# Kernel tuning notes

Measured on AMD Instinct MI355X. Metric: run time of the kernel, lower is better.

The kernel has to match this reference:

```python
import jax, jax.numpy as jnp
import numpy as np

EPS = 1e-4
HEADS = 8
DIM_HEAD = 32
BALANCE = 0.3


def _normalize(x, dims):
    # torch normalize(): norm over `dims` in fp32; norm = eps + norm*sqrt(norm.numel()/x.numel())
    red = 1
    for d in dims:
        red *= x.shape[d]
    norm = jnp.sqrt(jnp.sum(jnp.square(x.astype(jnp.float32)), axis=dims, keepdims=True))
    norm = EPS + norm / np.sqrt(red)
    return x / norm.astype(x.dtype)


def _mpconv1x1(x, w, gain=1.0):
    # MPConv forward (eval mode): weight-normalize per output channel, scale, 1x1 conv
    w = w.astype(jnp.float32)
    w = _normalize(w, (1, 2, 3))
    fan_in = w.shape[1] * w.shape[2] * w.shape[3]
    w = (w * (gain / np.sqrt(fan_in))).astype(x.dtype)[:, :, 0, 0]  # [out, in]
    return jnp.einsum('oi,nihw->nohw', w, x)


def setup_inputs() -> dict:
    key = jax.random.key(0)
    k1, k2, k3 = jax.random.split(key, 3)
    x = jax.random.normal(k1, (2, 256, 48, 48), dtype=jnp.float32)
    w_qkv = jax.random.normal(k2, (768, 256, 1, 1), dtype=jnp.float32)
    w_out = jax.random.normal(k3, (256, 256, 1, 1), dtype=jnp.float32)
    return {"x": x, "w_qkv": w_qkv, "w_out": w_out}


def reference(x, w_qkv, w_out):
    n, c, h, w_sp = x.shape
    seq = h * w_sp
    y = _mpconv1x1(x, w_qkv)                          # [n, 3c, h, w]
    y = y.reshape(n, HEADS, DIM_HEAD, 3, seq)         # channel split: head x dim_head x 3
    y = _normalize(y, (2,))                           # L2-normalize over dim_head axis
    q = y[:, :, :, 0, :]
    k = y[:, :, :, 1, :]
    v = y[:, :, :, 2, :]
    # scores [n, h, q, k] with k scaled by 1/sqrt(dim_head)
    att = jax.nn.softmax(jnp.einsum('nhcq,nhck->nhqk', q, k) / np.sqrt(DIM_HEAD), axis=3)
    y = jnp.einsum('nhqk,nhck->nhcq', att, v)         # [n, heads, dim_head, seq]
    y = _mpconv1x1(y.reshape(n, c, h, w_sp), w_out)
    t = BALANCE
    # mp_sum: lerp then magnitude-preserving rescale
    return (x + t * (y - x)) / np.sqrt((1 - t) ** 2 + t ** 2)
```

## Files before the change

### kernel.cpp

```cpp
#include <hip/hip_runtime.h>
#include <math.h>

#define EPSN 1e-4f
#define SEQ 2304

using bf16x8 = __attribute__((ext_vector_type(8))) short;
using f32x4  = __attribute__((ext_vector_type(4))) float;

__device__ inline unsigned short f2bf(float x) {
    union { float f; unsigned u; } c; c.f = x;
    unsigned u = c.u;
    u += 0x7fffu + ((u >> 16) & 1u);
    return (unsigned short)(u >> 16);
}

__device__ inline unsigned cvt_pk_bf16(float lo, float hi) {
    unsigned r;
    asm("v_cvt_pk_bf16_f32 %0, %1, %2" : "=v"(r) : "v"(lo), "v"(hi));
    return r;
}
__device__ inline void permlane32_swap(unsigned &a, unsigned &b) {
    asm("v_permlane32_swap_b32 %0, %1" : "+v"(a), "+v"(b));
}
__device__ inline void permlane16_swap(unsigned &a, unsigned &b) {
    asm("v_permlane16_swap_b32 %0, %1" : "+v"(a), "+v"(b));
}

__global__ __launch_bounds__(256) void prep_w_kernel(const float* __restrict__ w_qkv,
                                                     const float* __restrict__ w_out,
                                                     unsigned short* __restrict__ wqb,
                                                     unsigned short* __restrict__ wob) {
    int wave = threadIdx.x >> 6, lane = threadIdx.x & 63;
    int row = blockIdx.x * 4 + wave;
    const float* src;
    unsigned short* dst;
    if (row < 768) { src = w_qkv + (size_t)row * 256; dst = wqb + (size_t)row * 256; }
    else           { src = w_out + (size_t)(row - 768) * 256; dst = wob + (size_t)(row - 768) * 256; }
    float4 v = *(const float4*)&src[lane * 4];
    float ss = v.x * v.x + v.y * v.y + v.z * v.z + v.w * v.w;
    for (int off = 32; off > 0; off >>= 1) ss += __shfl_xor(ss, off, 64);
    float sc = 1.0f / (sqrtf(ss) + 16.0f * EPSN);
    unsigned p0 = (unsigned)f2bf(v.x * sc) | ((unsigned)f2bf(v.y * sc) << 16);
    unsigned p1 = (unsigned)f2bf(v.z * sc) | ((unsigned)f2bf(v.w * sc) << 16);
    *(uint2*)&dst[lane * 4] = make_uint2(p0, p1);
}

__global__ __launch_bounds__(256) void qkv_fused_kernel(const float* __restrict__ x,
                                                        const unsigned short* __restrict__ wqb,
                                                        unsigned short* __restrict__ qn,
                                                        unsigned short* __restrict__ kn,
                                                        unsigned short* __restrict__ vn) {
    __shared__ __align__(16) unsigned short Xs[32][264];
    __shared__ float Cs[96][33];
    __shared__ __align__(16) unsigned short Vls[32][40];
    int bid = blockIdx.x;
    int xcd = bid & 7, j = bid >> 3;
    int h = j & 7;
    int tile = xcd * 18 + (j >> 3);
    int st2 = tile % 72, n = tile / 72;
    int tid = threadIdx.x;
    int wave = tid >> 6, lane = tid & 63;
    int ln = lane & 15, quad = lane >> 4;
    int sgrp = wave & 1, mgrp = wave >> 1;
    int s0 = st2 * 32;

    {
        int ci = tid >> 3, sv = (tid & 7) * 4;
#pragma unroll
        for (int p = 0; p < 8; ++p) {
            int c = p * 32 + ci;
            float4 v = *(const float4*)&x[(size_t)(n * 256 + c) * SEQ + s0 + sv];
            Xs[sv + 0][c] = f2bf(v.x);
            Xs[sv + 1][c] = f2bf(v.y);
            Xs[sv + 2][c] = f2bf(v.z);
            Xs[sv + 3][c] = f2bf(v.w);
        }
    }
    __syncthreads();

    const unsigned short* Abase = wqb + (size_t)(h * 96 + mgrp * 48 + ln) * 256 + quad * 8;
    f32x4 acc[3];
#pragma unroll
    for (int m = 0; m < 3; ++m) acc[m] = (f32x4){0.f, 0.f, 0.f, 0.f};
#pragma unroll
    for (int kc = 0; kc < 8; ++kc) {
        bf16x8 b = *(const bf16x8*)&Xs[sgrp * 16 + ln][kc * 32 + quad * 8];
#pragma unroll
        for (int m = 0; m < 3; ++m) {
            bf16x8 a = *(const bf16x8*)(Abase + (size_t)(m * 16) * 256 + kc * 32);
            acc[m] = __builtin_amdgcn_mfma_f32_16x16x32_bf16(a, b, acc[m], 0, 0, 0);
        }
    }
#pragma unroll
    for (int m = 0; m < 3; ++m)
#pragma unroll
        for (int r = 0; r < 4; ++r)
            Cs[mgrp * 48 + m * 16 + quad * 4 + r][sgrp * 16 + ln] = acc[m][r];
    __syncthreads();
    int nh = n * 8 + h;
    if (tid < 96) {
        int sl = tid & 31, wh = tid >> 5;
        int s = st2 * 32 + sl;
        float v[32];
        float ss = 0.f;
#pragma unroll
        for (int d = 0; d < 32; ++d) { v[d] = Cs[3 * d + wh][sl]; ss += v[d] * v[d]; }
        float inv = 1.0f / (EPSN + sqrtf(ss * (1.0f / 32.0f)));
        if (wh == 0) inv *= 0.17677669529663687f * 1.4426950408889634f;
        if (wh == 2) {
#pragma unroll
            for (int d = 0; d < 32; ++d) Vls[d][sl] = f2bf(v[d] * inv);
        } else {
            unsigned short* dst = (wh == 1 ? kn : qn) + (size_t)nh * 73728 + (size_t)s * 32;
            unsigned wbuf[16];
#pragma unroll
            for (int j2 = 0; j2 < 16; ++j2)
                wbuf[j2] = (unsigned)f2bf(v[2 * j2] * inv) | ((unsigned)f2bf(v[2 * j2 + 1] * inv) << 16);
#pragma unroll
            for (int j2 = 0; j2 < 4; ++j2) {
                uint4 t4 = make_uint4(wbuf[4 * j2], wbuf[4 * j2 + 1], wbuf[4 * j2 + 2], wbuf[4 * j2 + 3]);
                *(uint4*)(dst + j2 * 8) = t4;
            }
        }
    }
    __syncthreads();
    {
        int d = tid >> 3, sj = (tid & 7) * 4;
        uint2 t2 = *(const uint2*)&Vls[d][sj];
        *(uint2*)&vn[(size_t)nh * 73728 + (size_t)d * SEQ + st2 * 32 + sj] = t2;
    }
}

__global__ __launch_bounds__(256) void attn_mfma_kernel(const unsigned short* __restrict__ qn,
                                                        const unsigned short* __restrict__ kn,
                                                        const unsigned short* __restrict__ vn,
                                                        float* __restrict__ Opart,
                                                        float* __restrict__ Lpart) {
    __shared__ __align__(16) unsigned short Ks[2][64][40];
    __shared__ __align__(16) unsigned short Vs[2][32][72];
    int tid = threadIdx.x;
    int wq = tid >> 6, lane = tid & 63;
    int ln = lane & 15, quad = lane >> 4;
    int bid = blockIdx.x;
    int xcd = bid & 7, bi = bid >> 3;
    int nh = xcd * 2 + (bi >= 144);
    int bi2 = (bi >= 144) ? bi - 144 : bi;
    int qt = bi2 % 36, kz = bi2 / 36;
    const unsigned short* Qg = qn + (size_t)nh * 73728;
    const unsigned short* Kg = kn + (size_t)nh * 73728;
    const unsigned short* Vg = vn + (size_t)nh * 73728;

    bf16x8 qf = *(const bf16x8*)(Qg + (size_t)(qt * 64 + wq * 16 + ln) * 32 + quad * 8);
    bf16x8 ones;
#pragma unroll
    for (int i = 0; i < 8; ++i) ones[i] = (short)0x3F80;

    f32x4 o0 = {0.f, 0.f, 0.f, 0.f};
    f32x4 o1 = {0.f, 0.f, 0.f, 0.f};
    f32x4 lac = {0.f, 0.f, 0.f, 0.f};

    const int NT = 9;
    int s0 = kz * NT * 64;

    auto compute_tile = [&](int bsel) {
        const f32x4 zero = {0.f, 0.f, 0.f, 0.f};
        unsigned w[4][2];
#pragma unroll
        for (int c = 0; c < 4; ++c) {
            bf16x8 kf = *(const bf16x8*)(&Ks[bsel][c * 16 + ln][quad * 8]);
            f32x4 sc = __builtin_amdgcn_mfma_f32_16x16x32_bf16(kf, qf, zero, 0, 0, 0);
            w[c][0] = cvt_pk_bf16(exp2f(sc[0]), exp2f(sc[1]));
            w[c][1] = cvt_pk_bf16(exp2f(sc[2]), exp2f(sc[3]));
        }
#pragma unroll
        for (int kc = 0; kc < 2; ++kc) {
            unsigned a0 = w[2 * kc][0], b0 = w[2 * kc + 1][0];
            permlane32_swap(a0, b0);
            permlane16_swap(a0, b0);
            unsigned a1 = w[2 * kc][1], b1 = w[2 * kc + 1][1];
            permlane32_swap(a1, b1);
            permlane16_swap(a1, b1);
            union { unsigned u[4]; bf16x8 v8; } pk;
            pk.u[0] = a0; pk.u[1] = a1; pk.u[2] = b0; pk.u[3] = b1;
            bf16x8 v0 = *(const bf16x8*)(&Vs[bsel][ln][kc * 32 + quad * 8]);
            bf16x8 v1 = *(const bf16x8*)(&Vs[bsel][16 + ln][kc * 32 + quad * 8]);
            lac = __builtin_amdgcn_mfma_f32_16x16x32_bf16(pk.v8, ones, lac, 0, 0, 0);
            o0  = __builtin_amdgcn_mfma_f32_16x16x32_bf16(pk.v8, v0, o0, 0, 0, 0);
            o1  = __builtin_amdgcn_mfma_f32_16x16x32_bf16(pk.v8, v1, o1, 0, 0, 0);
        }
    };

    uint4 kA = *(const uint4*)(Kg + (size_t)s0 * 32 + tid * 8);
    uint4 vA = *(const uint4*)(Vg + (size_t)(tid >> 3) * SEQ + s0 + (tid & 7) * 8);
    *(uint4*)(&Ks[0][tid >> 2][(tid & 3) * 8]) = kA;
    *(uint4*)(&Vs[0][tid >> 3][(tid & 7) * 8]) = vA;
    uint4 kB = *(const uint4*)(Kg + (size_t)(s0 + 64) * 32 + tid * 8);
    uint4 vB = *(const uint4*)(Vg + (size_t)(tid >> 3) * SEQ + (s0 + 64) + (tid & 7) * 8);

    for (int i = 0; i < NT; i += 2) {
        if (i + 2 < NT) {
            int sn = s0 + (i + 2) * 64;
            kA = *(const uint4*)(Kg + (size_t)sn * 32 + tid * 8);
            vA = *(const uint4*)(Vg + (size_t)(tid >> 3) * SEQ + sn + (tid & 7) * 8);
        }
        __syncthreads();
        compute_tile(0);
        if (i + 1 < NT) {
            *(uint4*)(&Ks[1][tid >> 2][(tid & 3) * 8]) = kB;
            *(uint4*)(&Vs[1][tid >> 3][(tid & 7) * 8]) = vB;
        }
        if (i + 3 < NT) {
            int sn = s0 + (i + 3) * 64;
            kB = *(const uint4*)(Kg + (size_t)sn * 32 + tid * 8);
            vB = *(const uint4*)(Vg + (size_t)(tid >> 3) * SEQ + sn + (tid & 7) * 8);
        }
        __syncthreads();
        if (i + 1 < NT) compute_tile(1);
        if (i + 2 < NT) {
            *(uint4*)(&Ks[0][tid >> 2][(tid & 3) * 8]) = kA;
            *(uint4*)(&Vs[0][tid >> 3][(tid & 7) * 8]) = vA;
        }
    }

    float* Ob = Opart + ((size_t)(kz * 16 + nh) * 36 + qt) * 2048;
    float* Lb = Lpart + ((size_t)(kz * 16 + nh) * 36 + qt) * 64;
#pragma unroll
    for (int r = 0; r < 4; ++r) {
        int ql = wq * 16 + quad * 4 + r;
        Ob[ql * 32 + ln]      = o0[r];
        Ob[ql * 32 + 16 + ln] = o1[r];
        if (ln == 0) Lb[ql] = lac[r];
    }
}

__global__ __launch_bounds__(256) void out_gemm_kernel(const float* __restrict__ Opart,
                                                       const float* __restrict__ Lpart,
                                                       const unsigned short* __restrict__ wob,
                                                       const float* __restrict__ x,
                                                       float* __restrict__ out) {
    __shared__ float Linv[8][16];
    __shared__ __align__(16) unsigned short Ys[16][264];
    int bid = blockIdx.x;
    int xcd = bid & 7, j = bid >> 3;
    int mt = j & 3;
    int u = j >> 2;
    int n = u & 1;
    int st = xcd * 18 + (u >> 1);
    int qt = st >> 2;
    int qo = (st & 3) * 16;
    int tid = threadIdx.x;

    if (tid < 128) {
        int h = tid >> 4, qi = tid & 15;
        size_t base = ((size_t)((n * 8 + h) * 36) + qt) * 64 + qo + qi;
        const size_t kzs = (size_t)16 * 36 * 64;
        float l = Lpart[base] + Lpart[base + kzs] + Lpart[base + 2 * kzs] + Lpart[base + 3 * kzs];
        Linv[h][qi] = 1.0f / l;
    }
    __syncthreads();
    {
        int qi = tid >> 4, dp = tid & 15, d0 = dp * 2;
        const size_t kzs = (size_t)16 * 36 * 2048;
#pragma unroll
        for (int h = 0; h < 8; ++h) {
            size_t ob = ((size_t)((n * 8 + h) * 36) + qt) * 2048 + (size_t)(qo + qi) * 32 + d0;
            float2 a = *(const float2*)&Opart[ob];
            float2 b = *(const float2*)&Opart[ob + kzs];
            float2 e = *(const float2*)&Opart[ob + 2 * kzs];
            float2 f = *(const float2*)&Opart[ob + 3 * kzs];
            float li = Linv[h][qi];
            float r0 = ((a.x + b.x) + (e.x + f.x)) * li;
            float r1 = ((a.y + b.y) + (e.y + f.y)) * li;
            *(unsigned*)&Ys[qi][h * 32 + d0] = cvt_pk_bf16(r0, r1);
        }
    }
    __syncthreads();

    int wave = tid >> 6, lane = tid & 63;
    int ln = lane & 15, quad = lane >> 4;
    int m0 = mt * 64 + wave * 16;
    const unsigned short* Abase = wob + (size_t)(m0 + ln) * 256 + quad * 8;
    f32x4 acc = (f32x4){0.f, 0.f, 0.f, 0.f};
#pragma unroll
    for (int kc = 0; kc < 8; ++kc) {
        bf16x8 a = *(const bf16x8*)(Abase + kc * 32);
        bf16x8 b = *(const bf16x8*)&Ys[ln][kc * 32 + quad * 8];
        acc = __builtin_amdgcn_mfma_f32_16x16x32_bf16(a, b, acc, 0, 0, 0);
    }
    const float c0f = 0.7f * 1.3130643285972254f;
    const float c1f = 0.3f * 1.3130643285972254f;
#pragma unroll
    for (int r = 0; r < 4; ++r) {
        int o = m0 + quad * 4 + r;
        int s = st * 16 + ln;
        size_t idx = (size_t)(n * 256 + o) * SEQ + s;
        out[idx] = c0f * x[idx] + c1f * acc[r];
    }
}

extern "C" void kernel_launch(void* const* d_in, const int* in_sizes, int n_in,
                              void* d_out, int out_size, void* d_ws, size_t ws_size,
                              hipStream_t stream) {
    (void)in_sizes; (void)n_in; (void)out_size; (void)ws_size;
    const float* x     = (const float*)d_in[0];
    const float* w_qkv = (const float*)d_in[1];
    const float* w_out = (const float*)d_in[2];
    float* out = (float*)d_out;
    float* ws  = (float*)d_ws;
    unsigned short* wqb = (unsigned short*)(ws);
    unsigned short* wob = (unsigned short*)(ws + 98304);
    unsigned short* qn  = (unsigned short*)(ws + 131072);
    unsigned short* kn  = (unsigned short*)(ws + 720896);
    unsigned short* vn  = (unsigned short*)(ws + 1310720);
    float* Opart = ws + 1900544;
    float* Lpart = ws + 6619136;

    hipLaunchKernelGGL(prep_w_kernel, dim3(256), dim3(256), 0, stream,
                       w_qkv, w_out, wqb, wob);
    hipLaunchKernelGGL(qkv_fused_kernel, dim3(1152), dim3(256), 0, stream,
                       x, wqb, qn, kn, vn);
    hipLaunchKernelGGL(attn_mfma_kernel, dim3(2304), dim3(256), 0, stream,
                       qn, kn, vn, Opart, Lpart);
    hipLaunchKernelGGL(out_gemm_kernel, dim3(1152), dim3(256), 0, stream,
                       Opart, Lpart, wob, x, out);
}
```

Before: 123.3 us.

## Load K/V fragments directly from global memory, dropping LDS double buffering

The attention kernel no longer stages K and V tiles through double-buffered shared memory with barriers. Each lane now reads its MFMA K and V fragments straight from global memory, relying on L1/L2 caching, since all four waves read the same K/V data. This removes LDS writes, reads and __syncthreads, but each wave now issues redundant global loads and loses the explicit prefetch overlap, so load latency may be exposed.

```diff
diff --git a/kernel.cpp b/kernel.cpp
--- a/kernel.cpp
+++ b/kernel.cpp
@@ -136,8 +136,6 @@
                                                         const unsigned short* __restrict__ vn,
                                                         float* __restrict__ Opart,
                                                         float* __restrict__ Lpart) {
-    __shared__ __align__(16) unsigned short Ks[2][64][40];
-    __shared__ __align__(16) unsigned short Vs[2][32][72];
     int tid = threadIdx.x;
     int wq = tid >> 6, lane = tid & 63;
     int ln = lane & 15, quad = lane >> 4;
@@ -162,12 +160,15 @@
     const int NT = 9;
     int s0 = kz * NT * 64;
 
-    auto compute_tile = [&](int bsel) {
+    const unsigned short* Kb = Kg + (size_t)(s0 + ln) * 32 + quad * 8;
+    const unsigned short* Vb = Vg + (size_t)ln * SEQ + s0 + quad * 8;
+
+    for (int i = 0; i < NT; ++i) {
         const f32x4 zero = {0.f, 0.f, 0.f, 0.f};
         unsigned w[4][2];
 #pragma unroll
         for (int c = 0; c < 4; ++c) {
-            bf16x8 kf = *(const bf16x8*)(&Ks[bsel][c * 16 + ln][quad * 8]);
+            bf16x8 kf = *(const bf16x8*)(Kb + (size_t)(i * 64 + c * 16) * 32);
             f32x4 sc = __builtin_amdgcn_mfma_f32_16x16x32_bf16(kf, qf, zero, 0, 0, 0);
             w[c][0] = cvt_pk_bf16(exp2f(sc[0]), exp2f(sc[1]));
             w[c][1] = cvt_pk_bf16(exp2f(sc[2]), exp2f(sc[3]));
@@ -182,43 +183,11 @@
             permlane16_swap(a1, b1);
             union { unsigned u[4]; bf16x8 v8; } pk;
             pk.u[0] = a0; pk.u[1] = a1; pk.u[2] = b0; pk.u[3] = b1;
-            bf16x8 v0 = *(const bf16x8*)(&Vs[bsel][ln][kc * 32 + quad * 8]);
-            bf16x8 v1 = *(const bf16x8*)(&Vs[bsel][16 + ln][kc * 32 + quad * 8]);
+            bf16x8 v0 = *(const bf16x8*)(Vb + i * 64 + kc * 32);
+            bf16x8 v1 = *(const bf16x8*)(Vb + (size_t)16 * SEQ + i * 64 + kc * 32);
             lac = __builtin_amdgcn_mfma_f32_16x16x32_bf16(pk.v8, ones, lac, 0, 0, 0);
             o0  = __builtin_amdgcn_mfma_f32_16x16x32_bf16(pk.v8, v0, o0, 0, 0, 0);
             o1  = __builtin_amdgcn_mfma_f32_16x16x32_bf16(pk.v8, v1, o1, 0, 0, 0);
-        }
-    };
-
-    uint4 kA = *(const uint4*)(Kg + (size_t)s0 * 32 + tid * 8);
-    uint4 vA = *(const uint4*)(Vg + (size_t)(tid >> 3) * SEQ + s0 + (tid & 7) * 8);
-    *(uint4*)(&Ks[0][tid >> 2][(tid & 3) * 8]) = kA;
-    *(uint4*)(&Vs[0][tid >> 3][(tid & 7) * 8]) = vA;
-    uint4 kB = *(const uint4*)(Kg + (size_t)(s0 + 64) * 32 + tid * 8);
-    uint4 vB = *(const uint4*)(Vg + (size_t)(tid >> 3) * SEQ + (s0 + 64) + (tid & 7) * 8);
-
-    for (int i = 0; i < NT; i += 2) {
-        if (i + 2 < NT) {
-            int sn = s0 + (i + 2) * 64;
-            kA = *(const uint4*)(Kg + (size_t)sn * 32 + tid * 8);
-            vA = *(const uint4*)(Vg + (size_t)(tid >> 3) * SEQ + sn + (tid & 7) * 8);
-        }
-        __syncthreads();
-        compute_tile(0);
-        if (i + 1 < NT) {
-            *(uint4*)(&Ks[1][tid >> 2][(tid & 3) * 8]) = kB;
-            *(uint4*)(&Vs[1][tid >> 3][(tid & 7) * 8]) = vB;
-        }
-        if (i + 3 < NT) {
-            int sn = s0 + (i + 3) * 64;
-            kB = *(const uint4*)(Kg + (size_t)sn * 32 + tid * 8);
-            vB = *(const uint4*)(Vg + (size_t)(tid >> 3) * SEQ + sn + (tid & 7) * 8);
-        }
-        __syncthreads();
-        if (i + 1 < NT) compute_tile(1);
-        if (i + 2 < NT) {
-            *(uint4*)(&Ks[0][tid >> 2][(tid & 3) * 8]) = kA;
-            *(uint4*)(&Vs[0][tid >> 3][(tid & 7) * 8]) = vA;
         }
     }
 
```

Result: slower. 151.4 us (+22.8%).
